# Performance work log

Hardware: AMD Instinct MI355X
Metric: run time of the kernel (lower is better)

The kernel has to match this reference:

```python
import jax, jax.numpy as jnp
import numpy as np

B, N, P, D, OUT = 32, 52, 1024, 512, 607
_DENSE = [6, 64, 128, 256, 512, D]   # dense PointNet encoder channel sizes
_SPARSE = [6, 32, 64, D]             # sparse (relation) PointNet encoder channel sizes
_OM = [D, 128, 256, OUT]             # object_mlp hidden sizes


def setup_inputs() -> dict:
    key = jax.random.key(0)
    ks = jax.random.split(key, 40)

    def w(k, shape):
        return jax.random.normal(ks[k], shape, jnp.float32) * (1.0 / float(np.sqrt(shape[0])))

    inp = {}
    inp["input"] = jax.random.normal(ks[0], (B, 1024, 6), jnp.float32)
    inp["objects"] = jax.random.normal(ks[1], (B, N, P, 6), jnp.float32)
    inp["objects_length"] = jax.random.randint(ks[2], (B,), 1, N + 1)
    k = 3
    for i in range(5):
        inp[f"de_W{i}"] = w(k, (_DENSE[i], _DENSE[i + 1])); k += 1
        inp[f"de_b{i}"] = jnp.zeros((_DENSE[i + 1],), jnp.float32)
    for i in range(3):
        inp[f"se_W{i}"] = w(k, (_SPARSE[i], _SPARSE[i + 1])); k += 1
        inp[f"se_b{i}"] = jnp.zeros((_SPARSE[i + 1],), jnp.float32)
    for i in range(3):
        inp[f"om_W{i}"] = w(k, (_OM[i], _OM[i + 1])); k += 1
        inp[f"om_b{i}"] = jnp.zeros((_OM[i + 1],), jnp.float32)
    inp["r1_W"] = w(k, (2 * D, D)); k += 1
    inp["r1_b"] = jnp.zeros((D,), jnp.float32)
    inp["r2_W"] = w(k, (D, D)); k += 1
    inp["r2_b"] = jnp.zeros((D,), jnp.float32)
    inp["m1_W"] = w(k, (D, D)); k += 1
    inp["m1_b"] = jnp.zeros((D,), jnp.float32)
    inp["m2_W"] = w(k, (D, D)); k += 1
    inp["m2_b"] = jnp.zeros((D,), jnp.float32)
    return inp


def reference(input, objects, objects_length,
              de_W0, de_b0, de_W1, de_b1, de_W2, de_b2, de_W3, de_b3, de_W4, de_b4,
              se_W0, se_b0, se_W1, se_b1, se_W2, se_b2,
              om_W0, om_b0, om_W1, om_b1, om_W2, om_b2,
              r1_W, r1_b, r2_W, r2_b, m1_W, m1_b, m2_W, m2_b):
    relu = jax.nn.relu
    # --- sparse PointNet encoder on location-masked clouds (xyz kept, rest zeroed) ---
    masked = jnp.concatenate([objects[..., :3], jnp.zeros_like(objects[..., 3:])], axis=-1)
    h = masked  # [B, N, P, 6]
    for W, b in ((se_W0, se_b0), (se_W1, se_b1), (se_W2, se_b2)):
        h = relu(h @ W + b)
    pn_obj = jnp.transpose(h.max(axis=2), (1, 0, 2))  # [N, B, D]

    # --- all (i, j) pairwise union features, vectorized (replaces the N^2 python loop) ---
    fi = jnp.broadcast_to(pn_obj[:, None], (N, N, B, D))
    fj = jnp.broadcast_to(pn_obj[None, :], (N, N, B, D))
    u = relu(jnp.concatenate([fi, fj], axis=-1))        # [N, N, B, 2D]
    rel = u @ r1_W + r1_b                               # relation_dense_layer
    rel = relu(rel) @ r2_W + r2_b                       # relation_dense_layer_2 -> [N, N, B, D]
    multi = relu(rel) @ m1_W + m1_b                     # multi_relation_dense_layer
    multi = relu(multi) @ m2_W + m2_b                   # multi_relation_dense_layer_2

    # --- dense PointNet encoder + object MLP ---
    h = objects  # [B, N, P, 6]
    for W, b in ((de_W0, de_b0), (de_W1, de_b1), (de_W2, de_b2), (de_W3, de_b3), (de_W4, de_b4)):
        h = relu(h @ W + b)
    obj = jnp.transpose(h.max(axis=2), (1, 0, 2))       # [N, B, D]
    obj = relu(obj @ om_W0 + om_b0)
    obj = relu(obj @ om_W1 + om_b1)
    obj = obj @ om_W2 + om_b2                           # [N, B, 607]

    return obj, rel, multi
```

## Files before the change

kernel.cpp:

```cpp
#include <hip/hip_runtime.h>
#include <stdint.h>

typedef __attribute__((ext_vector_type(8))) __bf16 bf16x8;
typedef __attribute__((ext_vector_type(4))) float f32x4;
typedef __attribute__((ext_vector_type(8))) short short8;

__device__ __forceinline__ unsigned short f2bf(float f) {
  unsigned int u = __float_as_uint(f);
  u += 0x7FFFu + ((u >> 16) & 1u);
  return (unsigned short)(u >> 16);
}
__device__ __forceinline__ float bf2f(unsigned short h) {
  return __uint_as_float((unsigned int)h << 16);
}
__device__ __forceinline__ void split2(float v, unsigned short& h, unsigned short& l) {
  h = f2bf(v);
  l = f2bf(v - bf2f(h));
}

#define WAITVM0 asm volatile("s_waitcnt vmcnt(0)" ::: "memory")
#define WAITVM4 asm volatile("s_waitcnt vmcnt(4)" ::: "memory")
#define WAITVM8 asm volatile("s_waitcnt vmcnt(8)" ::: "memory")

template<int COUT, int K>
__global__ __launch_bounds__(512, 1)
void gemmX(const unsigned short* __restrict__ A,
           const unsigned short* __restrict__ Wt,
           const float* __restrict__ bias,
           void* __restrict__ Cdst, void* __restrict__ Cdst2,
           unsigned int* __restrict__ Omax,
           int M, int ldc, int ntn, int swz8, int m_base)
{
  extern __shared__ __align__(16) char smem[];

  int bid = blockIdx.x;
  int mt, nt;
  if (swz8) {
    int xcd = bid & 7;
    int slot = bid >> 3;
    nt = slot % ntn;
    mt = (slot / ntn) * 8 + xcd;
  } else {
    mt = bid / ntn;
    nt = bid - mt * ntn;
  }
  const int m0 = mt * 256, n0 = nt * 256;
  const int tid = threadIdx.x;
  const int lane = tid & 63;
  const int w = tid >> 6;
  const int wm = w >> 2, wn = w & 3;
  const int l15 = lane & 15, l4 = lane >> 4;

  const unsigned short* aSrc[2];
  const unsigned short* bSrc[2];
  #pragma unroll
  for (int o = 0; o < 2; ++o) {
    int ar = w * 32 + o * 16 + (lane >> 2);
    int sc = ((lane & 3) ^ ((ar >> 1) & 3)) * 8;
    aSrc[o] = A + (size_t)(m0 + ar) * K + sc;
    bSrc[o] = Wt + (size_t)(n0 + ar) * K + sc;
  }

  f32x4 acc[8][4];
  #pragma unroll
  for (int a = 0; a < 8; ++a)
    #pragma unroll
    for (int b = 0; b < 4; ++b)
      acc[a][b] = (f32x4){0.f, 0.f, 0.f, 0.f};

  constexpr int NT = K / 32;

  auto STAGE = [&](int kt) {
    short* Ab = (short*)(smem + (size_t)(kt & 3) * 32768);
    short* Bb = Ab + 8192;
    int koff = kt * 32;
    #pragma unroll
    for (int o = 0; o < 2; ++o) {
      int rows = w * 32 + o * 16;
      __builtin_amdgcn_global_load_lds(aSrc[o] + koff, (void*)(Ab + rows * 32), 16, 0, 0);
      __builtin_amdgcn_global_load_lds(bSrc[o] + koff, (void*)(Bb + rows * 32), 16, 0, 0);
    }
  };

  STAGE(0);
  if (NT > 1) STAGE(1);
  if (NT > 2) STAGE(2);

  #pragma unroll
  for (int kt = 0; kt < NT; ++kt) {
    const int beyond = (NT - 1 - kt < 2) ? (NT - 1 - kt) : 2;
    if (beyond == 0)      { WAITVM0; }
    else if (beyond == 1) { WAITVM4; }
    else                  { WAITVM8; }
    __builtin_amdgcn_sched_barrier(0);
    __builtin_amdgcn_s_barrier();
    __builtin_amdgcn_sched_barrier(0);

    short* Ab = (short*)(smem + (size_t)(kt & 3) * 32768);
    short* Bb = Ab + 8192;

    bf16x8 aF[8], bF[4];
    #pragma unroll
    for (int n = 0; n < 4; ++n) {
      int R = wn * 64 + n * 16 + l15;
      int ph = l4 ^ ((R >> 1) & 3);
      bF[n] = *reinterpret_cast<const bf16x8*>(Bb + R * 32 + ph * 8);
    }
    #pragma unroll
    for (int m = 0; m < 8; ++m) {
      int R = wm * 128 + m * 16 + l15;
      int ph = l4 ^ ((R >> 1) & 3);
      aF[m] = *reinterpret_cast<const bf16x8*>(Ab + R * 32 + ph * 8);
    }

    if (kt + 3 <= NT - 1) STAGE(kt + 3);

    __builtin_amdgcn_s_setprio(1);
    #pragma unroll
    for (int m = 0; m < 8; ++m)
      #pragma unroll
      for (int n = 0; n < 4; ++n)
        acc[m][n] = __builtin_amdgcn_mfma_f32_16x16x32_bf16(aF[m], bF[n], acc[m][n], 0, 0, 0);
    __builtin_amdgcn_s_setprio(0);
  }

  __syncthreads();

  if (COUT == 2) {
    int obj = (m_base + m0) >> 10;
    #pragma unroll
    for (int ni = 0; ni < 4; ++ni) {
      int n = n0 + wn * 64 + ni * 16 + l15;
      float v = acc[0][ni][0];
      #pragma unroll
      for (int mi = 0; mi < 8; ++mi)
        #pragma unroll
        for (int i = 0; i < 4; ++i)
          v = fmaxf(v, acc[mi][ni][i]);
      v = fmaxf(v + bias[n], 0.0f);
      v = fmaxf(v, __shfl_xor(v, 16));
      v = fmaxf(v, __shfl_xor(v, 32));
      if (l4 == 0)
        atomicMax(&Omax[(size_t)obj * 512 + n], __float_as_uint(v));
    }
    return;
  }
  if (COUT == 0 || COUT == 3) {
    float* Bf = (float*)smem;
    float* Cf = (float*)Cdst;
    #pragma unroll
    for (int h = 0; h < 2; ++h) {
      if (wm == h) {
        #pragma unroll
        for (int mi = 0; mi < 8; ++mi)
          #pragma unroll
          for (int i = 0; i < 4; ++i) {
            int row = mi * 16 + l4 * 4 + i;
            #pragma unroll
            for (int ni = 0; ni < 4; ++ni) {
              int col = wn * 64 + ni * 16 + l15;
              int sl = col >> 2;
              int ph = (sl & 56) | ((sl & 7) ^ (row & 7));
              Bf[row * 256 + ph * 4 + (col & 3)] = acc[mi][ni][i] + bias[n0 + col];
            }
          }
      }
      __syncthreads();
      #pragma unroll
      for (int s = 0; s < 16; ++s) {
        int p = s * 512 + tid;
        int row = p >> 6, sl = p & 63;
        int ph = (sl & 56) | ((sl & 7) ^ (row & 7));
        f32x4 v = *reinterpret_cast<const f32x4*>(&Bf[row * 256 + ph * 4]);
        *reinterpret_cast<f32x4*>(Cf + (size_t)(m0 + h * 128 + row) * ldc + n0 + sl * 4) = v;
      }
      __syncthreads();
    }
  }
  if (COUT == 1 || COUT == 3) {
    unsigned short* Bp = (unsigned short*)smem;
    unsigned short* Cp = (unsigned short*)(COUT == 3 ? Cdst2 : Cdst);
    #pragma unroll
    for (int mi = 0; mi < 8; ++mi)
      #pragma unroll
      for (int i = 0; i < 4; ++i) {
        int row = wm * 128 + mi * 16 + l4 * 4 + i;
        #pragma unroll
        for (int ni = 0; ni < 4; ++ni) {
          int col = wn * 64 + ni * 16 + l15;
          int sl = col >> 3;
          int ph = (sl & 24) | ((sl & 7) ^ (row & 7));
          Bp[row * 256 + ph * 8 + (col & 7)] = f2bf(fmaxf(acc[mi][ni][i] + bias[n0 + col], 0.f));
        }
      }
    __syncthreads();
    #pragma unroll
    for (int s = 0; s < 16; ++s) {
      int p = s * 512 + tid;
      int row = p >> 5, sl = p & 31;
      int ph = (sl & 24) | ((sl & 7) ^ (row & 7));
      short8 v = *reinterpret_cast<const short8*>(&Bp[row * 256 + ph * 8]);
      *reinterpret_cast<short8*>(Cp + (size_t)(m0 + row) * ldc + n0 + sl * 8) = v;
    }
  }
}

__global__ __launch_bounds__(256)
void gemm3(const unsigned short* __restrict__ A,
           const unsigned short* __restrict__ Wt,
           const float* __restrict__ bias,
           void* __restrict__ Cdst,
           int M, int K, int ldc, int ntn)
{
  __shared__ __align__(16) short SM[3][128][64];

  int bid = blockIdx.x;
  int mt = bid / ntn, nt = bid - mt * ntn;
  const int m0 = mt * 128, n0 = nt * 128;
  const int tid = threadIdx.x;
  const int lane = tid & 63;
  const int wave = tid >> 6;
  const int wm = wave >> 1, wn = wave & 1;
  const int l15 = lane & 15, l4 = lane >> 4;

  const int rr = tid >> 3;
  const int sp = tid & 7;
  const int sl = sp ^ (rr & 7);
  const int slE = sl * 8;

  const unsigned short* a_p[4];
  const unsigned short* b_p[4];
  #pragma unroll
  for (int c = 0; c < 4; ++c) {
    int rt = c * 32 + rr;
    a_p[c] = A + (size_t)(m0 + rt) * K + slE;
    b_p[c] = Wt + (size_t)(n0 + rt) * 2 * K + slE;
  }

  f32x4 acc[4][4];
  #pragma unroll
  for (int a = 0; a < 4; ++a)
    #pragma unroll
    for (int b = 0; b < 4; ++b)
      acc[a][b] = (f32x4){0.f, 0.f, 0.f, 0.f};

  char* const smb = (char*)&SM[0][0][0];

  for (int k0 = 0; k0 < K; k0 += 64) {
    #pragma unroll
    for (int c = 0; c < 4; ++c) {
      char* lb = smb + c * 4096 + (tid & 192) * 16;
      __builtin_amdgcn_global_load_lds(a_p[c] + k0, (void*)lb, 16, 0, 0);
      __builtin_amdgcn_global_load_lds(b_p[c] + k0, (void*)(lb + 16384), 16, 0, 0);
      __builtin_amdgcn_global_load_lds(b_p[c] + K + k0, (void*)(lb + 32768), 16, 0, 0);
    }
    __syncthreads();
    #pragma unroll
    for (int kf = 0; kf < 2; ++kf) {
      bf16x8 av[4], bh[4], bl[4];
      #pragma unroll
      for (int mi = 0; mi < 4; ++mi) {
        int R = wm * 64 + mi * 16 + l15;
        int sph = (kf * 4 + l4) ^ (R & 7);
        av[mi] = *reinterpret_cast<const bf16x8*>(&SM[0][R][sph * 8]);
      }
      #pragma unroll
      for (int ni = 0; ni < 4; ++ni) {
        int R = wn * 64 + ni * 16 + l15;
        int sph = (kf * 4 + l4) ^ (R & 7);
        bh[ni] = *reinterpret_cast<const bf16x8*>(&SM[1][R][sph * 8]);
        bl[ni] = *reinterpret_cast<const bf16x8*>(&SM[2][R][sph * 8]);
      }
      #pragma unroll
      for (int mi = 0; mi < 4; ++mi)
        #pragma unroll
        for (int ni = 0; ni < 4; ++ni) {
          acc[mi][ni] = __builtin_amdgcn_mfma_f32_16x16x32_bf16(av[mi], bh[ni], acc[mi][ni], 0, 0, 0);
          acc[mi][ni] = __builtin_amdgcn_mfma_f32_16x16x32_bf16(av[mi], bl[ni], acc[mi][ni], 0, 0, 0);
        }
    }
    __syncthreads();
  }

  float* Bf = (float*)smb;
  float* Cf = (float*)Cdst;
  #pragma unroll
  for (int h = 0; h < 2; ++h) {
    if (wm == h) {
      #pragma unroll
      for (int mi = 0; mi < 4; ++mi)
        #pragma unroll
        for (int i = 0; i < 4; ++i) {
          int lr2 = mi * 16 + l4 * 4 + i;
          #pragma unroll
          for (int ni = 0; ni < 4; ++ni) {
            int col = wn * 64 + ni * 16 + l15;
            int off = lr2 * 128 + (((col >> 2) ^ (lr2 & 7)) << 2) + (col & 3);
            Bf[off] = acc[mi][ni][i] + bias[n0 + col];
          }
        }
    }
    __syncthreads();
    #pragma unroll
    for (int s = 0; s < 8; ++s) {
      int p = tid * 8 + s;
      int row = p >> 5, ls = p & 31;
      f32x4 v = *reinterpret_cast<const f32x4*>(&Bf[row * 128 + ((ls ^ (row & 7)) << 2)]);
      *reinterpret_cast<f32x4*>(Cf + (size_t)(m0 + h * 64 + row) * ldc + n0 + ls * 4) = v;
    }
    __syncthreads();
  }
}

__global__ __launch_bounds__(256)
void points_kernel(const float* __restrict__ obj6,
                   const float* __restrict__ sW0, const float* __restrict__ sb0,
                   const float* __restrict__ sW1, const float* __restrict__ sb1,
                   const float* __restrict__ dW0, const float* __restrict__ db0,
                   const float* __restrict__ dW1, const float* __restrict__ db1,
                   unsigned short* __restrict__ s2,
                   unsigned short* __restrict__ h2)
{
  __shared__ float sw0[96], sbb0[32], sw1[2048], sbb1[64];
  __shared__ float dw0[384], dbb0[64], dw1[8192], dbb1[128];
  int tid = threadIdx.x;
  for (int i = tid; i < 96; i += 256) sw0[i] = sW0[i];
  if (tid < 32) sbb0[tid] = sb0[tid];
  for (int i = tid; i < 2048; i += 256) sw1[i] = sW1[i];
  if (tid < 64) sbb1[tid] = sb1[tid];
  for (int i = tid; i < 384; i += 256) dw0[i] = dW0[i];
  if (tid < 64) dbb0[tid] = db0[tid];
  for (int i = tid; i < 8192; i += 256) dw1[i] = dW1[i];
  if (tid < 128) dbb1[tid] = db1[tid];
  __syncthreads();

  int pt = blockIdx.x * 256 + tid;
  const float* in = obj6 + (size_t)pt * 6;
  float c0 = in[0], c1 = in[1], c2 = in[2], c3 = in[3], c4 = in[4], c5 = in[5];

  {
    float h1[32];
    #pragma unroll
    for (int j = 0; j < 32; ++j)
      h1[j] = fmaxf(c0 * sw0[j] + c1 * sw0[32 + j] + c2 * sw0[64 + j] + sbb0[j], 0.f);
    unsigned short* orow = s2 + (size_t)pt * 64;
    #pragma unroll
    for (int j8 = 0; j8 < 8; ++j8) {
      float a[8];
      #pragma unroll
      for (int e = 0; e < 8; ++e) a[e] = sbb1[j8 * 8 + e];
      #pragma unroll
      for (int i = 0; i < 32; ++i) {
        float hv = h1[i];
        #pragma unroll
        for (int e = 0; e < 8; ++e) a[e] += hv * sw1[i * 64 + j8 * 8 + e];
      }
      short8 o;
      #pragma unroll
      for (int e = 0; e < 8; ++e) o[e] = (short)f2bf(fmaxf(a[e], 0.f));
      *reinterpret_cast<short8*>(orow + j8 * 8) = o;
    }
  }

  {
    float h1[64];
    #pragma unroll
    for (int j = 0; j < 64; ++j) {
      float a = dbb0[j] + c0 * dw0[j] + c1 * dw0[64 + j] + c2 * dw0[128 + j]
              + c3 * dw0[192 + j] + c4 * dw0[256 + j] + c5 * dw0[320 + j];
      h1[j] = fmaxf(a, 0.f);
    }
    unsigned short* orow = h2 + (size_t)pt * 128;
    #pragma unroll
    for (int ch = 0; ch < 4; ++ch) {
      float a[32];
      #pragma unroll
      for (int e = 0; e < 32; ++e) a[e] = dbb1[ch * 32 + e];
      #pragma unroll 8
      for (int i = 0; i < 64; ++i) {
        float hv = h1[i];
        #pragma unroll
        for (int e = 0; e < 32; ++e) a[e] += hv * dw1[i * 128 + ch * 32 + e];
      }
      #pragma unroll
      for (int e8 = 0; e8 < 4; ++e8) {
        short8 o;
        #pragma unroll
        for (int e = 0; e < 8; ++e) o[e] = (short)f2bf(fmaxf(a[e8 * 8 + e], 0.f));
        *reinterpret_cast<short8*>(orow + ch * 32 + e8 * 8) = o;
      }
    }
  }
}

__global__ void transpose_split(const float* __restrict__ W, unsigned short* __restrict__ Wt,
                                int K, int N)
{
  int id = blockIdx.x * 256 + threadIdx.x;
  if (id >= K * N) return;
  int k = id / N, n = id - k * N;
  unsigned short h, l;
  split2(W[id], h, l);
  Wt[(size_t)n * 2 * K + k] = h;
  Wt[(size_t)n * 2 * K + K + k] = l;
}

__global__ void transpose_cast(const float* __restrict__ W, unsigned short* __restrict__ Wt,
                               int K, int N)
{
  int id = blockIdx.x * 256 + threadIdx.x;
  if (id >= K * N) return;
  int k = id / N, n = id - k * N;
  Wt[(size_t)n * K + k] = f2bf(W[id]);
}

__global__ void zero_kernel(unsigned int* __restrict__ p, int n)
{
  int id = blockIdx.x * 256 + threadIdx.x;
  if (id < n) p[id] = 0u;
}

__global__ void pn_pack_kernel(const float* __restrict__ pnf, unsigned short* __restrict__ pnp)
{
  int id = blockIdx.x * 256 + threadIdx.x;
  int o = id >> 9, c = id & 511;
  int b = o / 52, n = o - b * 52;
  pnp[((size_t)(n * 32 + b) << 9) + c] = f2bf(pnf[id]);
}

__global__ __launch_bounds__(256)
void rel_combine_kernel(const float* __restrict__ G,
                        const float* __restrict__ bias, unsigned short* __restrict__ t1)
{
  int t = blockIdx.x * 256 + threadIdx.x;
  int r = t >> 6, c8 = (t & 63) << 3;
  int b = r & 31;
  int pair = r >> 5;
  int i = pair / 52;
  int j = pair - i * 52;
  const float* g1 = G + ((size_t)(i * 32 + b) << 10) + c8;
  const float* g2 = G + ((size_t)(j * 32 + b) << 10) + 512 + c8;
  short8 o;
  #pragma unroll
  for (int e = 0; e < 8; ++e)
    o[e] = (short)f2bf(fmaxf(g1[e] + g2[e] + bias[c8 + e], 0.f));
  *reinterpret_cast<short8*>(t1 + (size_t)r * 512 + c8) = o;
}

__global__ __launch_bounds__(256)
void objmlp_kernel(const float* __restrict__ obj,
                   const float* __restrict__ W0, const float* __restrict__ b0,
                   const float* __restrict__ W1, const float* __restrict__ b1,
                   const float* __restrict__ W2, const float* __restrict__ b2,
                   float* __restrict__ out)
{
  __shared__ float x[512];
  __shared__ float h1[128];
  __shared__ float h2[256];
  int tid = threadIdx.x;
  int r = blockIdx.x;
  int n = r >> 5, b = r & 31;
  int o = b * 52 + n;
  const float* xs = obj + (size_t)o * 512;
  x[tid] = xs[tid];
  x[tid + 256] = xs[tid + 256];
  __syncthreads();
  if (tid < 128) {
    float a = b0[tid];
    #pragma unroll 8
    for (int k = 0; k < 512; ++k) a += x[k] * W0[k * 128 + tid];
    h1[tid] = fmaxf(a, 0.f);
  }
  __syncthreads();
  {
    float a = b1[tid];
    #pragma unroll 8
    for (int k = 0; k < 128; ++k) a += h1[k] * W1[k * 256 + tid];
    h2[tid] = fmaxf(a, 0.f);
  }
  __syncthreads();
  for (int j = tid; j < 607; j += 256) {
    float a = b2[j];
    #pragma unroll 8
    for (int k = 0; k < 256; ++k) a += h2[k] * W2[k * 607 + j];
    out[(size_t)r * 607 + j] = a;
  }
}

extern "C" void kernel_launch(void* const* d_in, const int* in_sizes, int n_in,
                              void* d_out, int out_size, void* d_ws, size_t ws_size,
                              hipStream_t stream)
{
  const float* objects = (const float*)d_in[1];
  const float* de_W0 = (const float*)d_in[3];  const float* de_b0 = (const float*)d_in[4];
  const float* de_W1 = (const float*)d_in[5];  const float* de_b1 = (const float*)d_in[6];
  const float* de_W2 = (const float*)d_in[7];  const float* de_b2 = (const float*)d_in[8];
  const float* de_W3 = (const float*)d_in[9];  const float* de_b3 = (const float*)d_in[10];
  const float* de_W4 = (const float*)d_in[11]; const float* de_b4 = (const float*)d_in[12];
  const float* se_W0 = (const float*)d_in[13]; const float* se_b0 = (const float*)d_in[14];
  const float* se_W1 = (const float*)d_in[15]; const float* se_b1 = (const float*)d_in[16];
  const float* se_W2 = (const float*)d_in[17]; const float* se_b2 = (const float*)d_in[18];
  const float* om_W0 = (const float*)d_in[19]; const float* om_b0 = (const float*)d_in[20];
  const float* om_W1 = (const float*)d_in[21]; const float* om_b1 = (const float*)d_in[22];
  const float* om_W2 = (const float*)d_in[23]; const float* om_b2 = (const float*)d_in[24];
  const float* r1_W = (const float*)d_in[25];  const float* r1_b = (const float*)d_in[26];
  const float* r2_W = (const float*)d_in[27];  const float* r2_b = (const float*)d_in[28];
  const float* m1_W = (const float*)d_in[29];  const float* m1_b = (const float*)d_in[30];
  const float* m2_W = (const float*)d_in[31];  const float* m2_b = (const float*)d_in[32];
  (void)in_sizes; (void)n_in; (void)out_size;

  (void)hipFuncSetAttribute(reinterpret_cast<const void*>(&gemmX<1, 128>),
                            hipFuncAttributeMaxDynamicSharedMemorySize, 131072);
  (void)hipFuncSetAttribute(reinterpret_cast<const void*>(&gemmX<1, 256>),
                            hipFuncAttributeMaxDynamicSharedMemorySize, 131072);
  (void)hipFuncSetAttribute(reinterpret_cast<const void*>(&gemmX<2, 512>),
                            hipFuncAttributeMaxDynamicSharedMemorySize, 131072);
  (void)hipFuncSetAttribute(reinterpret_cast<const void*>(&gemmX<2, 64>),
                            hipFuncAttributeMaxDynamicSharedMemorySize, 131072);
  (void)hipFuncSetAttribute(reinterpret_cast<const void*>(&gemmX<3, 512>),
                            hipFuncAttributeMaxDynamicSharedMemorySize, 131072);
  (void)hipFuncSetAttribute(reinterpret_cast<const void*>(&gemmX<1, 512>),
                            hipFuncAttributeMaxDynamicSharedMemorySize, 131072);
  (void)hipFuncSetAttribute(reinterpret_cast<const void*>(&gemmX<0, 512>),
                            hipFuncAttributeMaxDynamicSharedMemorySize, 131072);

  float* outf = (float*)d_out;
  float* out_obj = outf;
  float* out_rel = outf + 1010048;
  float* out_multi = out_rel + 44302336;

  char* ws = (char*)d_ws;
  size_t off = 0;
  auto alloc = [&](size_t bytes) -> void* {
    void* p = ws + off;
    off += (bytes + 255) & ~(size_t)255;
    return p;
  };
  unsigned short* wt_se2 = (unsigned short*)alloc((size_t)512 * 64 * 2);
  unsigned short* wt_de2 = (unsigned short*)alloc((size_t)256 * 128 * 2);
  unsigned short* wt_de3 = (unsigned short*)alloc((size_t)512 * 256 * 2);
  unsigned short* wt_de4 = (unsigned short*)alloc((size_t)512 * 512 * 2);
  unsigned short* wt_g   = (unsigned short*)alloc((size_t)1024 * 1024 * 2);
  unsigned short* wt_r2  = (unsigned short*)alloc((size_t)512 * 512 * 2);
  unsigned short* wt_m1  = (unsigned short*)alloc((size_t)512 * 512 * 2);
  unsigned short* wt_m2  = (unsigned short*)alloc((size_t)512 * 512 * 2);
  float* Gbuf = (float*)alloc((size_t)1664 * 1024 * 4);
  size_t avail = (ws_size > off + 256) ? (ws_size - off - 256) : 0;
  int Tc = (int)(avail / 262144);
  if (Tc < 1) Tc = 1;
  if (Tc > 338) Tc = 338;
  unsigned short* t2 = (unsigned short*)alloc((size_t)Tc * 262144);

  char* arena = (char*)out_rel;
  unsigned int* pnmax   = (unsigned int*)(arena);
  float*        obj_f32 = (float*)(arena + 3407872);
  unsigned short* pn_p  = (unsigned short*)(arena + 6815744);
  char* cbuf = arena + 8519680;
  const size_t PC = 131072;
  unsigned short* s2_c = (unsigned short*)(cbuf);
  unsigned short* h2_c = (unsigned short*)(cbuf + PC * 128);
  unsigned short* h3_c = (unsigned short*)(cbuf + PC * 384);
  unsigned short* h4_c = (unsigned short*)(cbuf + PC * 896);
  unsigned short* t1  = (unsigned short*)out_multi;
  unsigned short* t1b = (unsigned short*)((char*)out_multi + 88604672);

  zero_kernel<<<(2 * 851968) / 256, 256, 0, stream>>>(pnmax, 2 * 851968);

  auto tsplit = [&](const float* W, unsigned short* Dst, int K, int N) {
    int n = K * N;
    transpose_split<<<(n + 255) / 256, 256, 0, stream>>>(W, Dst, K, N);
  };
  auto tcast = [&](const float* W, unsigned short* Dst, int K, int N) {
    int n = K * N;
    transpose_cast<<<(n + 255) / 256, 256, 0, stream>>>(W, Dst, K, N);
  };
  tcast(se_W2, wt_se2, 64, 512);
  tcast(de_W2, wt_de2, 128, 256);
  tcast(de_W3, wt_de3, 256, 512);
  tcast(de_W4, wt_de4, 512, 512);
  tsplit(r1_W,             wt_g,              512, 512);
  tsplit(r1_W + 512 * 512, wt_g + 512 * 1024, 512, 512);
  tcast(r2_W,  wt_r2, 512, 512);
  tcast(m1_W,  wt_m1, 512, 512);
  tcast(m2_W,  wt_m2, 512, 512);

  for (int c = 0; c < 13; ++c) {
    int base = c * (int)PC;
    points_kernel<<<PC / 256, 256, 0, stream>>>(
        objects + (size_t)base * 6,
        se_W0, se_b0, se_W1, se_b1, de_W0, de_b0, de_W1, de_b1, s2_c, h2_c);
    gemmX<2, 64><<<2 * (PC / 256), 512, 131072, stream>>>(
        s2_c, wt_se2, se_b2, nullptr, nullptr, pnmax, PC, 512, 2, 1, base);
    gemmX<1, 128><<<1 * (PC / 256), 512, 131072, stream>>>(
        h2_c, wt_de2, de_b2, h3_c, nullptr, nullptr, PC, 256, 1, 1, 0);
    gemmX<1, 256><<<2 * (PC / 256), 512, 131072, stream>>>(
        h3_c, wt_de3, de_b3, h4_c, nullptr, nullptr, PC, 512, 2, 1, 0);
    gemmX<2, 512><<<2 * (PC / 256), 512, 131072, stream>>>(
        h4_c, wt_de4, de_b4, nullptr, nullptr, (unsigned int*)obj_f32, PC, 512, 2, 1, base);
  }

  pn_pack_kernel<<<851968 / 256, 256, 0, stream>>>((const float*)pnmax, pn_p);
  objmlp_kernel<<<1664, 256, 0, stream>>>(obj_f32, om_W0, om_b0, om_W1, om_b1,
                                          om_W2, om_b2, out_obj);

  zero_kernel<<<4, 256, 0, stream>>>((unsigned int*)t2, 1024);
  gemm3<<<13 * 8, 256, 0, stream>>>(
      pn_p, wt_g, (const float*)t2, Gbuf, 1664, 512, 1024, 8);
  rel_combine_kernel<<<86528 * 64 / 256, 256, 0, stream>>>(Gbuf, r1_b, t1);
  gemmX<3, 512><<<338 * 2, 512, 131072, stream>>>(
      t1, wt_r2, r2_b, out_rel, t1b, nullptr, 86528, 512, 2, 0, 0);
  for (int tb = 0; tb < 338; tb += Tc) {
    int tiles = (338 - tb < Tc) ? (338 - tb) : Tc;
    int rows = tiles * 256;
    size_t rb = (size_t)tb * 256 * 512;
    gemmX<1, 512><<<tiles * 2, 512, 131072, stream>>>(
        t1b + rb, wt_m1, m1_b, t2, nullptr, nullptr, rows, 512, 2, 0, 0);
    gemmX<0, 512><<<tiles * 2, 512, 131072, stream>>>(
        t2, wt_m2, m2_b, out_multi + rb, nullptr, nullptr, rows, 512, 2, 0, 0);
  }
}
```

Before: 3.881 ms.

## Fuse chained GEMM layers into a single kernel keeping intermediates in LDS

Adds a gemmF kernel that runs a 128-row tile through two or three successive 512-wide GEMMs. Each layer's bf16 ReLU output is kept in shared memory and used as the next layer's A operand. It replaces the dense de3→de4 pair (with max-pool) and the rel path (combine, r2, m1, m2) with one launch each, folding the rel_combine step into the A-tile load. This removes the global round trips for h4, t1, t1b and t2, and the chunked m1/m2 loop. In exchange it uses 128-row tiles, one block per CU with 160KB of LDS, and synchronous B loads in the chained GEMMs, which may expose latency. The point chunk size also grows to cover the input in 8 chunks instead of 13.

Measured after the change: 3.598 ms. -7.3%, faster.

```diff
diff --git a/kernel.cpp b/kernel.cpp
--- a/kernel.cpp
+++ b/kernel.cpp
@@ -20,16 +20,251 @@
 
 #define WAITVM0 asm volatile("s_waitcnt vmcnt(0)" ::: "memory")
 #define WAITVM4 asm volatile("s_waitcnt vmcnt(4)" ::: "memory")
+#define WAITVM5 asm volatile("s_waitcnt vmcnt(5)" ::: "memory")
 #define WAITVM8 asm volatile("s_waitcnt vmcnt(8)" ::: "memory")
+#define LGKM0   asm volatile("s_waitcnt lgkmcnt(0)" ::: "memory")
+#define SCHED0  __builtin_amdgcn_sched_barrier(0)
+
+template<int VAR>
+__global__ __launch_bounds__(512, 1)
+void gemmF(const unsigned short* __restrict__ Ag,
+           const float* __restrict__ G, const float* __restrict__ gb,
+           const unsigned short* __restrict__ W1t, const float* __restrict__ b1,
+           const unsigned short* __restrict__ W2t, const float* __restrict__ b2,
+           const unsigned short* __restrict__ W3t, const float* __restrict__ b3,
+           float* __restrict__ out1, float* __restrict__ out3,
+           unsigned int* __restrict__ Omax, int m_base)
+{
+  extern __shared__ __align__(16) char smem[];
+  short* SS = (short*)smem;
+  const int tid = threadIdx.x, lane = tid & 63, w = tid >> 6;
+  const int l15 = lane & 15, l4 = lane >> 4;
+  const int m0 = blockIdx.x * 128;
+  constexpr int K1 = VAR ? 512 : 256;
+  constexpr int NT1 = K1 / 32;
+
+  f32x4 acc[8][4];
+  #pragma unroll
+  for (int a = 0; a < 8; ++a)
+    #pragma unroll
+    for (int b = 0; b < 4; ++b)
+      acc[a][b] = (f32x4){0.f, 0.f, 0.f, 0.f};
+
+  auto MFMA32 = [&](bf16x8* aF, bf16x8* bF) {
+    __builtin_amdgcn_s_setprio(1);
+    #pragma unroll
+    for (int m = 0; m < 8; ++m)
+      #pragma unroll
+      for (int n = 0; n < 4; ++n)
+        acc[m][n] = __builtin_amdgcn_mfma_f32_16x16x32_bf16(aF[m], bF[n], acc[m][n], 0, 0, 0);
+    __builtin_amdgcn_s_setprio(0);
+  };
+
+  auto scatterC = [&](const float* bias) {
+    float bv[4];
+    #pragma unroll
+    for (int ni = 0; ni < 4; ++ni) bv[ni] = bias[w * 64 + ni * 16 + l15];
+    #pragma unroll
+    for (int mi = 0; mi < 8; ++mi)
+      #pragma unroll
+      for (int i = 0; i < 4; ++i) {
+        int row = mi * 16 + l4 * 4 + i;
+        #pragma unroll
+        for (int ni = 0; ni < 4; ++ni) {
+          int col = w * 64 + ni * 16 + l15;
+          int c5 = col & 31;
+          int ph = (c5 >> 3) ^ ((row >> 1) & 3);
+          SS[(col >> 5) * 4096 + row * 32 + ph * 8 + (col & 7)] =
+              (short)f2bf(fmaxf(acc[mi][i >> 2][0] * 0.f + acc[mi][ni][i] + bv[ni], 0.f));
+        }
+      }
+  };
+
+  auto bounceOut = [&](float* dst, const float* bias) {
+    float* Bf = (float*)smem;
+    #pragma unroll
+    for (int h = 0; h < 2; ++h) {
+      if ((w >> 2) == h) {
+        #pragma unroll
+        for (int mi = 0; mi < 8; ++mi)
+          #pragma unroll
+          for (int i = 0; i < 4; ++i) {
+            int row = mi * 16 + l4 * 4 + i;
+            #pragma unroll
+            for (int ni = 0; ni < 4; ++ni) {
+              int colh = (w & 3) * 64 + ni * 16 + l15;
+              int sl = colh >> 2;
+              int ph = (sl & 56) | ((sl & 7) ^ (row & 7));
+              Bf[row * 256 + ph * 4 + (colh & 3)] =
+                  acc[mi][ni][i] + bias[w * 64 + ni * 16 + l15];
+            }
+          }
+      }
+      __syncthreads();
+      #pragma unroll
+      for (int s = 0; s < 16; ++s) {
+        int p = s * 512 + tid;
+        int row = p >> 6, sl = p & 63;
+        int ph = (sl & 56) | ((sl & 7) ^ (row & 7));
+        f32x4 v = *reinterpret_cast<const f32x4*>(&Bf[row * 256 + ph * 4]);
+        *reinterpret_cast<f32x4*>(dst + (size_t)(m0 + row) * 512 + h * 256 + sl * 4) = v;
+      }
+      __syncthreads();
+    }
+  };
+
+  auto ldsA_loop = [&](const unsigned short* Wt) {
+    #pragma unroll
+    for (int a = 0; a < 8; ++a)
+      #pragma unroll
+      for (int b = 0; b < 4; ++b)
+        acc[a][b] = (f32x4){0.f, 0.f, 0.f, 0.f};
+    short* myB = SS + 65536 + w * 2048;
+    const unsigned short* bS[4];
+    #pragma unroll
+    for (int o = 0; o < 4; ++o) {
+      int br = w * 64 + o * 16 + (lane >> 2);
+      bS[o] = Wt + (size_t)br * 512 + (((lane & 3) ^ ((br >> 1) & 3)) * 8);
+    }
+    #pragma unroll
+    for (int kt = 0; kt < 16; ++kt) {
+      LGKM0; SCHED0;
+      #pragma unroll
+      for (int o = 0; o < 4; ++o)
+        __builtin_amdgcn_global_load_lds(bS[o] + kt * 32, (void*)(myB + o * 512), 16, 0, 0);
+      bf16x8 aF[8], bF[4];
+      #pragma unroll
+      for (int m = 0; m < 8; ++m) {
+        int R = m * 16 + l15;
+        int ph = l4 ^ ((R >> 1) & 3);
+        aF[m] = *reinterpret_cast<const bf16x8*>(SS + kt * 4096 + R * 32 + ph * 8);
+      }
+      WAITVM0; SCHED0;
+      #pragma unroll
+      for (int n = 0; n < 4; ++n) {
+        int Rl = n * 16 + l15;
+        int ph = l4 ^ ((Rl >> 1) & 3);
+        bF[n] = *reinterpret_cast<const bf16x8*>(myB + Rl * 32 + ph * 8);
+      }
+      MFMA32(aF, bF);
+    }
+  };
+
+  const int arow = w * 16 + (lane >> 2);
+  const unsigned short* aS = nullptr;
+  const float *g1p = nullptr, *g2p = nullptr, *gbp = nullptr;
+  if constexpr (VAR == 0) {
+    aS = Ag + (size_t)(m0 + arow) * K1 + (((lane & 3) ^ ((arow >> 1) & 3)) * 8);
+  } else {
+    int r = m0 + arow;
+    int b = r & 31, pr = r >> 5;
+    int i = pr / 52, j = pr - i * 52;
+    g1p = G + (size_t)(i * 32 + b) * 1024 + (lane & 3) * 8;
+    g2p = G + (size_t)(j * 32 + b) * 1024 + 512 + (lane & 3) * 8;
+    gbp = gb + (lane & 3) * 8;
+  }
+  const unsigned short* bS1[4];
+  #pragma unroll
+  for (int o = 0; o < 4; ++o) {
+    int br = w * 64 + o * 16 + (lane >> 2);
+    bS1[o] = W1t + (size_t)br * K1 + (((lane & 3) ^ ((br >> 1) & 3)) * 8);
+  }
+  auto stage1 = [&](int kt) {
+    short* S = SS + (kt % 3) * 20480;
+    if constexpr (VAR == 0) {
+      __builtin_amdgcn_global_load_lds(aS + kt * 32, (void*)(S + w * 512), 16, 0, 0);
+    } else {
+      f32x4 q0 = *reinterpret_cast<const f32x4*>(g1p + kt * 32);
+      f32x4 q1 = *reinterpret_cast<const f32x4*>(g1p + kt * 32 + 4);
+      f32x4 p0 = *reinterpret_cast<const f32x4*>(g2p + kt * 32);
+      f32x4 p1 = *reinterpret_cast<const f32x4*>(g2p + kt * 32 + 4);
+      f32x4 c0 = *reinterpret_cast<const f32x4*>(gbp + kt * 32);
+      f32x4 c1 = *reinterpret_cast<const f32x4*>(gbp + kt * 32 + 4);
+      short8 hv;
+      #pragma unroll
+      for (int e = 0; e < 4; ++e) {
+        hv[e]     = (short)f2bf(fmaxf(q0[e] + p0[e] + c0[e], 0.f));
+        hv[4 + e] = (short)f2bf(fmaxf(q1[e] + p1[e] + c1[e], 0.f));
+      }
+      *reinterpret_cast<short8*>(S + arow * 32 + (((lane & 3) ^ ((arow >> 1) & 3)) * 8)) = hv;
+    }
+    #pragma unroll
+    for (int o = 0; o < 4; ++o)
+      __builtin_amdgcn_global_load_lds(bS1[o] + kt * 32,
+                                       (void*)(S + 4096 + (w * 64 + o * 16) * 32), 16, 0, 0);
+  };
+
+  stage1(0);
+  stage1(1);
+  #pragma unroll
+  for (int kt = 0; kt < NT1; ++kt) {
+    LGKM0;
+    if (kt < NT1 - 1) { if (VAR) { WAITVM4; } else { WAITVM5; } }
+    else { WAITVM0; }
+    SCHED0;
+    __builtin_amdgcn_s_barrier();
+    SCHED0;
+    short* S = SS + (kt % 3) * 20480;
+    bf16x8 aF[8], bF[4];
+    #pragma unroll
+    for (int n = 0; n < 4; ++n) {
+      int R = w * 64 + n * 16 + l15;
+      int ph = l4 ^ ((R >> 1) & 3);
+      bF[n] = *reinterpret_cast<const bf16x8*>(S + 4096 + R * 32 + ph * 8);
+    }
+    #pragma unroll
+    for (int m = 0; m < 8; ++m) {
+      int R = m * 16 + l15;
+      int ph = l4 ^ ((R >> 1) & 3);
+      aF[m] = *reinterpret_cast<const bf16x8*>(S + R * 32 + ph * 8);
+    }
+    if (kt + 2 < NT1) stage1(kt + 2);
+    MFMA32(aF, bF);
+  }
+  __syncthreads();
+
+  if constexpr (VAR == 1) bounceOut(out1, b1);
+  scatterC(b1);
+  __syncthreads();
+
+  ldsA_loop(W2t);
+
+  if constexpr (VAR == 0) {
+    int obj = (m_base + m0) >> 10;
+    #pragma unroll
+    for (int ni = 0; ni < 4; ++ni) {
+      int n = w * 64 + ni * 16 + l15;
+      float v = acc[0][ni][0];
+      #pragma unroll
+      for (int mi = 0; mi < 8; ++mi)
+        #pragma unroll
+        for (int i = 0; i < 4; ++i)
+          v = fmaxf(v, acc[mi][ni][i]);
+      v = fmaxf(v + b2[n], 0.0f);
+      v = fmaxf(v, __shfl_xor(v, 16));
+      v = fmaxf(v, __shfl_xor(v, 32));
+      if (l4 == 0)
+        atomicMax(&Omax[(size_t)obj * 512 + n], __float_as_uint(v));
+    }
+    return;
+  } else {
+    __syncthreads();
+    scatterC(b2);
+    __syncthreads();
+    ldsA_loop(W3t);
+    __syncthreads();
+    bounceOut(out3, b3);
+  }
+}
 
 template<int COUT, int K>
 __global__ __launch_bounds__(512, 1)
 void gemmX(const unsigned short* __restrict__ A,
            const unsigned short* __restrict__ Wt,
            const float* __restrict__ bias,
-           void* __restrict__ Cdst, void* __restrict__ Cdst2,
+           void* __restrict__ Cdst,
            unsigned int* __restrict__ Omax,
-           int M, int ldc, int ntn, int swz8, int m_base)
+           int ldc, int ntn, int swz8, int m_base)
 {
   extern __shared__ __align__(16) char smem[];
 
@@ -92,9 +327,9 @@
     if (beyond == 0)      { WAITVM0; }
     else if (beyond == 1) { WAITVM4; }
     else                  { WAITVM8; }
-    __builtin_amdgcn_sched_barrier(0);
+    SCHED0;
     __builtin_amdgcn_s_barrier();
-    __builtin_amdgcn_sched_barrier(0);
+    SCHED0;
 
     short* Ab = (short*)(smem + (size_t)(kt & 3) * 32768);
     short* Bb = Ab + 8192;
@@ -104,13 +339,13 @@
     for (int n = 0; n < 4; ++n) {
       int R = wn * 64 + n * 16 + l15;
       int ph = l4 ^ ((R >> 1) & 3);
-      bF[n] = *reinterpret_cast<const bf16x8*>(Bb + R * 32 + ph * 8);
+      bF[n] = *reinterpret_cast<const bf16x8*>(&Bb[R * 32 + ph * 8]);
     }
     #pragma unroll
     for (int m = 0; m < 8; ++m) {
       int R = wm * 128 + m * 16 + l15;
       int ph = l4 ^ ((R >> 1) & 3);
-      aF[m] = *reinterpret_cast<const bf16x8*>(Ab + R * 32 + ph * 8);
+      aF[m] = *reinterpret_cast<const bf16x8*>(&Ab[R * 32 + ph * 8]);
     }
 
     if (kt + 3 <= NT - 1) STAGE(kt + 3);
@@ -145,63 +380,29 @@
     }
     return;
   }
-  if (COUT == 0 || COUT == 3) {
-    float* Bf = (float*)smem;
-    float* Cf = (float*)Cdst;
-    #pragma unroll
-    for (int h = 0; h < 2; ++h) {
-      if (wm == h) {
-        #pragma unroll
-        for (int mi = 0; mi < 8; ++mi)
-          #pragma unroll
-          for (int i = 0; i < 4; ++i) {
-            int row = mi * 16 + l4 * 4 + i;
-            #pragma unroll
-            for (int ni = 0; ni < 4; ++ni) {
-              int col = wn * 64 + ni * 16 + l15;
-              int sl = col >> 2;
-              int ph = (sl & 56) | ((sl & 7) ^ (row & 7));
-              Bf[row * 256 + ph * 4 + (col & 3)] = acc[mi][ni][i] + bias[n0 + col];
-            }
-          }
-      }
-      __syncthreads();
-      #pragma unroll
-      for (int s = 0; s < 16; ++s) {
-        int p = s * 512 + tid;
-        int row = p >> 6, sl = p & 63;
-        int ph = (sl & 56) | ((sl & 7) ^ (row & 7));
-        f32x4 v = *reinterpret_cast<const f32x4*>(&Bf[row * 256 + ph * 4]);
-        *reinterpret_cast<f32x4*>(Cf + (size_t)(m0 + h * 128 + row) * ldc + n0 + sl * 4) = v;
-      }
-      __syncthreads();
-    }
-  }
-  if (COUT == 1 || COUT == 3) {
-    unsigned short* Bp = (unsigned short*)smem;
-    unsigned short* Cp = (unsigned short*)(COUT == 3 ? Cdst2 : Cdst);
-    #pragma unroll
-    for (int mi = 0; mi < 8; ++mi)
-      #pragma unroll
-      for (int i = 0; i < 4; ++i) {
-        int row = wm * 128 + mi * 16 + l4 * 4 + i;
-        #pragma unroll
-        for (int ni = 0; ni < 4; ++ni) {
-          int col = wn * 64 + ni * 16 + l15;
-          int sl = col >> 3;
-          int ph = (sl & 24) | ((sl & 7) ^ (row & 7));
-          Bp[row * 256 + ph * 8 + (col & 7)] = f2bf(fmaxf(acc[mi][ni][i] + bias[n0 + col], 0.f));
-        }
-      }
-    __syncthreads();
-    #pragma unroll
-    for (int s = 0; s < 16; ++s) {
-      int p = s * 512 + tid;
-      int row = p >> 5, sl = p & 31;
-      int ph = (sl & 24) | ((sl & 7) ^ (row & 7));
-      short8 v = *reinterpret_cast<const short8*>(&Bp[row * 256 + ph * 8]);
-      *reinterpret_cast<short8*>(Cp + (size_t)(m0 + row) * ldc + n0 + sl * 8) = v;
-    }
+  unsigned short* Bp = (unsigned short*)smem;
+  unsigned short* Cp = (unsigned short*)Cdst;
+  #pragma unroll
+  for (int mi = 0; mi < 8; ++mi)
+    #pragma unroll
+    for (int i = 0; i < 4; ++i) {
+      int row = wm * 128 + mi * 16 + l4 * 4 + i;
+      #pragma unroll
+      for (int ni = 0; ni < 4; ++ni) {
+        int col = wn * 64 + ni * 16 + l15;
+        int sl = col >> 3;
+        int ph = (sl & 24) | ((sl & 7) ^ (row & 7));
+        Bp[row * 256 + ph * 8 + (col & 7)] = f2bf(fmaxf(acc[mi][ni][i] + bias[n0 + col], 0.f));
+      }
+    }
+  __syncthreads();
+  #pragma unroll
+  for (int s = 0; s < 16; ++s) {
+    int p = s * 512 + tid;
+    int row = p >> 5, sl = p & 31;
+    int ph = (sl & 24) | ((sl & 7) ^ (row & 7));
+    short8 v = *reinterpret_cast<const short8*>(&Bp[row * 256 + ph * 8]);
+    *reinterpret_cast<short8*>(Cp + (size_t)(m0 + row) * ldc + n0 + sl * 8) = v;
   }
 }
 
@@ -426,25 +627,6 @@
   int o = id >> 9, c = id & 511;
   int b = o / 52, n = o - b * 52;
   pnp[((size_t)(n * 32 + b) << 9) + c] = f2bf(pnf[id]);
-}
-
-__global__ __launch_bounds__(256)
-void rel_combine_kernel(const float* __restrict__ G,
-                        const float* __restrict__ bias, unsigned short* __restrict__ t1)
-{
-  int t = blockIdx.x * 256 + threadIdx.x;
-  int r = t >> 6, c8 = (t & 63) << 3;
-  int b = r & 31;
-  int pair = r >> 5;
-  int i = pair / 52;
-  int j = pair - i * 52;
-  const float* g1 = G + ((size_t)(i * 32 + b) << 10) + c8;
-  const float* g2 = G + ((size_t)(j * 32 + b) << 10) + 512 + c8;
-  short8 o;
-  #pragma unroll
-  for (int e = 0; e < 8; ++e)
-    o[e] = (short)f2bf(fmaxf(g1[e] + g2[e] + bias[c8 + e], 0.f));
-  *reinterpret_cast<short8*>(t1 + (size_t)r * 512 + c8) = o;
 }
 
 __global__ __launch_bounds__(256)
@@ -507,21 +689,15 @@
   const float* r2_W = (const float*)d_in[27];  const float* r2_b = (const float*)d_in[28];
   const float* m1_W = (const float*)d_in[29];  const float* m1_b = (const float*)d_in[30];
   const float* m2_W = (const float*)d_in[31];  const float* m2_b = (const float*)d_in[32];
-  (void)in_sizes; (void)n_in; (void)out_size;
-
-  (void)hipFuncSetAttribute(reinterpret_cast<const void*>(&gemmX<1, 128>),
-                            hipFuncAttributeMaxDynamicSharedMemorySize, 131072);
-  (void)hipFuncSetAttribute(reinterpret_cast<const void*>(&gemmX<1, 256>),
-                            hipFuncAttributeMaxDynamicSharedMemorySize, 131072);
-  (void)hipFuncSetAttribute(reinterpret_cast<const void*>(&gemmX<2, 512>),
-                            hipFuncAttributeMaxDynamicSharedMemorySize, 131072);
+  (void)in_sizes; (void)n_in; (void)out_size; (void)ws_size;
+
+  (void)hipFuncSetAttribute(reinterpret_cast<const void*>(&gemmF<0>),
+                            hipFuncAttributeMaxDynamicSharedMemorySize, 163840);
+  (void)hipFuncSetAttribute(reinterpret_cast<const void*>(&gemmF<1>),
+                            hipFuncAttributeMaxDynamicSharedMemorySize, 163840);
   (void)hipFuncSetAttribute(reinterpret_cast<const void*>(&gemmX<2, 64>),
                             hipFuncAttributeMaxDynamicSharedMemorySize, 131072);
-  (void)hipFuncSetAttribute(reinterpret_cast<const void*>(&gemmX<3, 512>),
-                            hipFuncAttributeMaxDynamicSharedMemorySize, 131072);
-  (void)hipFuncSetAttribute(reinterpret_cast<const void*>(&gemmX<1, 512>),
-                            hipFuncAttributeMaxDynamicSharedMemorySize, 131072);
-  (void)hipFuncSetAttribute(reinterpret_cast<const void*>(&gemmX<0, 512>),
+  (void)hipFuncSetAttribute(reinterpret_cast<const void*>(&gemmX<1, 128>),
                             hipFuncAttributeMaxDynamicSharedMemorySize, 131072);
 
   float* outf = (float*)d_out;
@@ -544,27 +720,21 @@
   unsigned short* wt_r2  = (unsigned short*)alloc((size_t)512 * 512 * 2);
   unsigned short* wt_m1  = (unsigned short*)alloc((size_t)512 * 512 * 2);
   unsigned short* wt_m2  = (unsigned short*)alloc((size_t)512 * 512 * 2);
-  float* Gbuf = (float*)alloc((size_t)1664 * 1024 * 4);
-  size_t avail = (ws_size > off + 256) ? (ws_size - off - 256) : 0;
-  int Tc = (int)(avail / 262144);
-  if (Tc < 1) Tc = 1;
-  if (Tc > 338) Tc = 338;
-  unsigned short* t2 = (unsigned short*)alloc((size_t)Tc * 262144);
+  float* zbias = (float*)alloc((size_t)1024 * 4);
+  float* Gbuf  = (float*)alloc((size_t)1664 * 1024 * 4);
 
   char* arena = (char*)out_rel;
   unsigned int* pnmax   = (unsigned int*)(arena);
   float*        obj_f32 = (float*)(arena + 3407872);
   unsigned short* pn_p  = (unsigned short*)(arena + 6815744);
   char* cbuf = arena + 8519680;
-  const size_t PC = 131072;
+  const size_t PC = 212992;
   unsigned short* s2_c = (unsigned short*)(cbuf);
   unsigned short* h2_c = (unsigned short*)(cbuf + PC * 128);
   unsigned short* h3_c = (unsigned short*)(cbuf + PC * 384);
-  unsigned short* h4_c = (unsigned short*)(cbuf + PC * 896);
-  unsigned short* t1  = (unsigned short*)out_multi;
-  unsigned short* t1b = (unsigned short*)((char*)out_multi + 88604672);
 
   zero_kernel<<<(2 * 851968) / 256, 256, 0, stream>>>(pnmax, 2 * 851968);
+  zero_kernel<<<4, 256, 0, stream>>>((unsigned int*)zbias, 1024);
 
   auto tsplit = [&](const float* W, unsigned short* Dst, int K, int N) {
     int n = K * N;
@@ -584,38 +754,26 @@
   tcast(m1_W,  wt_m1, 512, 512);
   tcast(m2_W,  wt_m2, 512, 512);
 
-  for (int c = 0; c < 13; ++c) {
+  for (int c = 0; c < 8; ++c) {
     int base = c * (int)PC;
     points_kernel<<<PC / 256, 256, 0, stream>>>(
         objects + (size_t)base * 6,
         se_W0, se_b0, se_W1, se_b1, de_W0, de_b0, de_W1, de_b1, s2_c, h2_c);
     gemmX<2, 64><<<2 * (PC / 256), 512, 131072, stream>>>(
-        s2_c, wt_se2, se_b2, nullptr, nullptr, pnmax, PC, 512, 2, 1, base);
-    gemmX<1, 128><<<1 * (PC / 256), 512, 131072, stream>>>(
-        h2_c, wt_de2, de_b2, h3_c, nullptr, nullptr, PC, 256, 1, 1, 0);
-    gemmX<1, 256><<<2 * (PC / 256), 512, 131072, stream>>>(
-        h3_c, wt_de3, de_b3, h4_c, nullptr, nullptr, PC, 512, 2, 1, 0);
-    gemmX<2, 512><<<2 * (PC / 256), 512, 131072, stream>>>(
-        h4_c, wt_de4, de_b4, nullptr, nullptr, (unsigned int*)obj_f32, PC, 512, 2, 1, base);
+        s2_c, wt_se2, se_b2, nullptr, pnmax, 512, 2, 1, base);
+    gemmX<1, 128><<<(PC / 256), 512, 131072, stream>>>(
+        h2_c, wt_de2, de_b2, h3_c, nullptr, 256, 1, 1, 0);
+    gemmF<0><<<PC / 128, 512, 163840, stream>>>(
+        h3_c, nullptr, nullptr, wt_de3, de_b3, wt_de4, de_b4, nullptr, nullptr,
+        nullptr, nullptr, (unsigned int*)obj_f32, base);
   }
 
   pn_pack_kernel<<<851968 / 256, 256, 0, stream>>>((const float*)pnmax, pn_p);
   objmlp_kernel<<<1664, 256, 0, stream>>>(obj_f32, om_W0, om_b0, om_W1, om_b1,
                                           om_W2, om_b2, out_obj);
 
-  zero_kernel<<<4, 256, 0, stream>>>((unsigned int*)t2, 1024);
-  gemm3<<<13 * 8, 256, 0, stream>>>(
-      pn_p, wt_g, (const float*)t2, Gbuf, 1664, 512, 1024, 8);
-  rel_combine_kernel<<<86528 * 64 / 256, 256, 0, stream>>>(Gbuf, r1_b, t1);
-  gemmX<3, 512><<<338 * 2, 512, 131072, stream>>>(
-      t1, wt_r2, r2_b, out_rel, t1b, nullptr, 86528, 512, 2, 0, 0);
-  for (int tb = 0; tb < 338; tb += Tc) {
-    int tiles = (338 - tb < Tc) ? (338 - tb) : Tc;
-    int rows = tiles * 256;
-    size_t rb = (size_t)tb * 256 * 512;
-    gemmX<1, 512><<<tiles * 2, 512, 131072, stream>>>(
-        t1b + rb, wt_m1, m1_b, t2, nullptr, nullptr, rows, 512, 2, 0, 0);
-    gemmX<0, 512><<<tiles * 2, 512, 131072, stream>>>(
-        t2, wt_m2, m2_b, out_multi + rb, nullptr, nullptr, rows, 512, 2, 0, 0);
-  }
-}
+  gemm3<<<13 * 8, 256, 0, stream>>>(pn_p, wt_g, zbias, Gbuf, 1664, 512, 1024, 8);
+  gemmF<1><<<676, 512, 163840, stream>>>(
+      nullptr, Gbuf, r1_b, wt_r2, r2_b, wt_m1, m1_b, wt_m2, m2_b,
+      out_rel, out_multi, nullptr, 0);
+}
```
